# Performance work log

Hardware: AMD Instinct MI355X
Metric: run time of the kernel (lower is better)

Reference implementation:

```python
import jax, jax.numpy as jnp
import numpy as np

B, S, H = 1, 2048, 2048
NH, NKV, HD = 16, 2, 128
ROPE_THETA = 1000000.0
BF16 = jnp.bfloat16


def setup_inputs() -> dict:
    key = jax.random.key(0)
    ks = jax.random.split(key, 6)
    hidden_states = jax.random.normal(ks[0], (B, S, H), dtype=jnp.float32)
    # causal additive mask, 0 on/below diagonal, large negative above
    causal = jnp.tril(jnp.ones((S, S), dtype=bool))
    attention_mask = jnp.where(causal, 0.0, -1e9).astype(jnp.float32)[None, None, :, :]
    position_ids = jnp.arange(S, dtype=jnp.int32)[None, :]
    sc = 1.0 / np.sqrt(H)
    Wq = jax.random.normal(ks[1], (H, H), dtype=jnp.float32) * sc
    bq = jnp.zeros((H,), dtype=jnp.float32)
    Wk = jax.random.normal(ks[2], (H, NKV * HD), dtype=jnp.float32) * sc
    bk = jnp.zeros((NKV * HD,), dtype=jnp.float32)
    Wv = jax.random.normal(ks[3], (H, NKV * HD), dtype=jnp.float32) * sc
    bv = jnp.zeros((NKV * HD,), dtype=jnp.float32)
    Wo = jax.random.normal(ks[4], (H, H), dtype=jnp.float32) * sc
    return {"hidden_states": hidden_states, "attention_mask": attention_mask,
            "position_ids": position_ids, "Wq": Wq, "bq": bq, "Wk": Wk, "bk": bk,
            "Wv": Wv, "bv": bv, "Wo": Wo}


def _rope_tables(pos):
    # pos: [S] int. freqs: [HD//2]
    freqs = 1.0 / (ROPE_THETA ** (jnp.arange(0, HD, 2, dtype=jnp.float32) / HD))
    ang = pos.astype(jnp.float32)[:, None] * freqs[None, :]  # [S, HD//2]
    return jnp.cos(ang), jnp.sin(ang)


def _apply_rope(x, cos, sin):
    # x: [B,S,nheads,HD]; cos/sin: [S,HD//2] -> broadcast over heads
    c = cos[None, :, None, :]
    s = sin[None, :, None, :]
    x1, x2 = x[..., : HD // 2], x[..., HD // 2 :]
    return jnp.concatenate([x1 * c - x2 * s, x1 * s + x2 * c], axis=-1)


def reference(hidden_states, attention_mask, position_ids, Wq, bq, Wk, bk, Wv, bv, Wo):
    x = hidden_states.astype(BF16)
    # bf16 projections (flax Dense dtype=bfloat16)
    q = (x @ Wq.astype(BF16) + bq.astype(BF16)).reshape(B, S, NH, HD)
    k = (x @ Wk.astype(BF16) + bk.astype(BF16)).reshape(B, S, NKV, HD)
    v = (x @ Wv.astype(BF16) + bv.astype(BF16)).reshape(B, S, NKV, HD)
    cos, sin = _rope_tables(position_ids[0])
    q = _apply_rope(q.astype(jnp.float32), cos, sin).astype(jnp.float32)
    k = _apply_rope(k.astype(jnp.float32), cos, sin).astype(jnp.float32)
    cache_k, cache_v = k, v  # cache holds un-repeated kv (k post-rope, v bf16)
    rep = NH // NKV  # GQA repeat
    k = jnp.repeat(k, rep, axis=2)
    vr = jnp.repeat(v, rep, axis=2)
    # [B,NH,S,HD]
    qh = q.transpose(0, 2, 1, 3)
    kh = k.transpose(0, 2, 1, 3)
    vh = vr.transpose(0, 2, 1, 3).astype(jnp.float32)
    scale = 1.0 / jnp.sqrt(jnp.float32(HD))
    scores = jnp.einsum('bhqd,bhkd->bhqk', qh, kh) * scale + attention_mask
    probs = jnp.clip(jax.nn.softmax(scores.astype(jnp.float32), axis=-1), 1e-09, 1 - 1e-09)
    attn = jnp.einsum('bhqk,bhkd->bhqd', probs, vh)
    attn = attn.transpose(0, 2, 1, 3).reshape(B, S, H)
    out = (attn.astype(BF16) @ Wo.astype(BF16)).astype(jnp.float32)
    return out, cache_k, cache_v
```

## Files before the change

kernel.cpp:

```cpp
#include <hip/hip_runtime.h>
#include <hip/hip_bf16.h>
#include <math.h>

#define S_LEN 2048
#define HDIM  2048
#define N_H   16
#define N_KV  2
#define HD_   128
#define NQKV  2560

typedef __attribute__((ext_vector_type(8))) short bf16x8;
typedef __attribute__((ext_vector_type(4))) float f32x4;
typedef __attribute__((ext_vector_type(16))) float f32x16;

#define GLDS16(gsrc, ldst)                                                      \
  __builtin_amdgcn_global_load_lds(                                             \
      (const __attribute__((address_space(1))) void*)(gsrc),                    \
      (__attribute__((address_space(3))) void*)(ldst), 16, 0, 0)

__device__ __forceinline__ ushort f2b(float x) {
  union { __hip_bfloat16 b; ushort u; } c;
  c.b = __float2bfloat16(x);
  return c.u;
}
__device__ __forceinline__ float b2f(ushort u) {
  union { float f; unsigned v; } c;
  c.v = ((unsigned)u) << 16;
  return c.f;
}
__device__ __forceinline__ uint pk2(float a, float b) {
  return (uint)f2b(a) | ((uint)f2b(b) << 16);
}

__global__ __launch_bounds__(256) void k_f32_to_bf16(const float* __restrict__ src,
                                                     ushort* __restrict__ dst, int n4) {
  int i = blockIdx.x * 256 + threadIdx.x;
  if (i >= n4) return;
  float4 v = ((const float4*)src)[i];
  ushort4 o;
  o.x = f2b(v.x); o.y = f2b(v.y); o.z = f2b(v.z); o.w = f2b(v.w);
  ((ushort4*)dst)[i] = o;
}

__global__ __launch_bounds__(256) void k_transpose_bf16(const float* __restrict__ src,
                                                        ushort* __restrict__ dst,
                                                        int R, int C) {
  __shared__ float t[64][65];
  int c0 = blockIdx.x * 64, r0 = blockIdx.y * 64;
  int tx = threadIdx.x & 63, ty = threadIdx.x >> 6;
#pragma unroll
  for (int i = 0; i < 16; ++i)
    t[i * 4 + ty][tx] = src[(size_t)(r0 + i * 4 + ty) * C + (c0 + tx)];
  __syncthreads();
#pragma unroll
  for (int i = 0; i < 16; ++i)
    dst[(size_t)(c0 + i * 4 + ty) * R + (r0 + tx)] = f2b(t[tx][i * 4 + ty]);
}

__global__ __launch_bounds__(256) void k_gemm_bt(const ushort* __restrict__ A,
                                                 const ushort* __restrict__ Bt,
                                                 ushort* __restrict__ Cp,
                                                 int M, int N, int Kfull, int Khalf) {
  __shared__ ushort lA[128 * 32];
  __shared__ ushort lB[128 * 32];
  const int tid = threadIdx.x;
  const int w = tid >> 6, lane = tid & 63;
  const int lr = lane & 15, lg = lane >> 4;
  const int bm = blockIdx.x * 128, bn = blockIdx.y * 128;
  const int wm = (w >> 1) * 64, wn = (w & 1) * 64;
  const int kbeg = blockIdx.z * Khalf;
  ushort* Cout = Cp + (size_t)blockIdx.z * M * N;
  f32x4 acc[4][4] = {};

  for (int k0 = kbeg; k0 < kbeg + Khalf; k0 += 32) {
    __syncthreads();
#pragma unroll
    for (int it = 0; it < 2; ++it) {
      const int idx = it * 256 + tid;
      const int row = idx >> 2;
      const int kc = (idx & 3) * 8;
      GLDS16(A + (size_t)(bm + row) * Kfull + k0 + kc, lA + (it * 4 + w) * 512);
      GLDS16(Bt + (size_t)(bn + row) * Kfull + k0 + kc, lB + (it * 4 + w) * 512);
    }
    __syncthreads();
    bf16x8 af[4], bf[4];
#pragma unroll
    for (int i = 0; i < 4; ++i) {
      af[i] = *(const bf16x8*)(lA + (wm + i * 16 + lr) * 32 + lg * 8);
      bf[i] = *(const bf16x8*)(lB + (wn + i * 16 + lr) * 32 + lg * 8);
    }
    __builtin_amdgcn_s_setprio(1);
#pragma unroll
    for (int mi = 0; mi < 4; ++mi)
#pragma unroll
      for (int ni = 0; ni < 4; ++ni)
        acc[mi][ni] =
            __builtin_amdgcn_mfma_f32_16x16x32_bf16(af[mi], bf[ni], acc[mi][ni], 0, 0, 0);
    __builtin_amdgcn_s_setprio(0);
  }

#pragma unroll
  for (int mi = 0; mi < 4; ++mi)
#pragma unroll
    for (int ni = 0; ni < 4; ++ni)
#pragma unroll
      for (int r = 0; r < 4; ++r) {
        const int row = bm + wm + mi * 16 + lg * 4 + r;
        const int col = bn + wn + ni * 16 + lr;
        Cout[(size_t)row * N + col] = f2b(acc[mi][ni][r]);
      }
}

__global__ __launch_bounds__(256) void k_epirope(const ushort* __restrict__ p0,
                                                 const ushort* __restrict__ p1,
                                                 const float* __restrict__ bq,
                                                 const float* __restrict__ bk,
                                                 const float* __restrict__ bv,
                                                 const int* __restrict__ pos_ids,
                                                 ushort* __restrict__ q_r,
                                                 ushort* __restrict__ k_r,
                                                 ushort* __restrict__ v_t,
                                                 float* __restrict__ cache_k,
                                                 float* __restrict__ cache_v) {
  const int s = blockIdx.x;
  const int t = threadIdx.x;
  __shared__ float row[NQKV];
  const uint* a = (const uint*)(p0 + (size_t)s * NQKV);
  const uint* b = (const uint*)(p1 + (size_t)s * NQKV);
#pragma unroll
  for (int j = 0; j < 5; ++j) {
    const int c2 = t + 256 * j;
    const uint u0 = a[c2], u1 = b[c2];
    const int c = 2 * c2;
    const float v0 = b2f((ushort)u0) + b2f((ushort)(u1 & 0xffff));
    const float v1 = b2f((ushort)(u0 >> 16)) + b2f((ushort)(u1 >> 16));
    const float bias0 = (c < 2048) ? bq[c] : (c < 2304 ? bk[c - 2048] : bv[c - 2304]);
    const float bias1 = (c + 1 < 2048) ? bq[c + 1]
                                       : (c + 1 < 2304 ? bk[c + 1 - 2048] : bv[c + 1 - 2304]);
    row[c] = b2f(f2b(b2f(f2b(v0)) + b2f(f2b(bias0))));
    row[c + 1] = b2f(f2b(b2f(f2b(v1)) + b2f(f2b(bias1))));
  }
  __syncthreads();

  const int i = t & 63, g = t >> 6;
  const float SCALE = 0.08838834764831845f;
  const float pos = (float)pos_ids[s];
  const float freq = (float)(1.0 / pow(1000000.0, (double)i / 64.0));
  float sn, cs;
  sincosf(pos * freq, &sn, &cs);

#pragma unroll
  for (int j = 0; j < 4; ++j) {
    const int h = j * 4 + g;
    const float x1 = row[h * 128 + i];
    const float x2 = row[h * 128 + 64 + i];
    const float o1 = x1 * cs - x2 * sn;
    const float o2 = x1 * sn + x2 * cs;
    const size_t qo = ((size_t)h * S_LEN + s) * 128;
    q_r[qo + i] = f2b(o1 * SCALE);
    q_r[qo + 64 + i] = f2b(o2 * SCALE);
  }
  if (g < 2) {
    const int kv = g;
    const float x1 = row[2048 + kv * 128 + i];
    const float x2 = row[2048 + kv * 128 + 64 + i];
    const float o1 = x1 * cs - x2 * sn;
    const float o2 = x1 * sn + x2 * cs;
    const size_t ko = ((size_t)kv * S_LEN + s) * 128;
    k_r[ko + i] = f2b(o1);
    k_r[ko + 64 + i] = f2b(o2);
    const size_t co = ((size_t)s * 2 + kv) * 128;
    cache_k[co + i] = o1;
    cache_k[co + 64 + i] = o2;
  }
  {
    const int kv = t >> 7, d = t & 127;
    const float vval = row[2304 + kv * 128 + d];
    cache_v[((size_t)s * 2 + kv) * 128 + d] = vval;
    v_t[((size_t)kv * 128 + d) * S_LEN + s] = f2b(vval);
  }
}

__global__ __launch_bounds__(256) void k_addround(const ushort* __restrict__ p0,
                                                  const ushort* __restrict__ p1,
                                                  float* __restrict__ out, int n2) {
  int i = blockIdx.x * 256 + threadIdx.x;
  if (i >= n2) return;
  const uint a = ((const uint*)p0)[i];
  const uint b = ((const uint*)p1)[i];
  float2 o;
  o.x = b2f(f2b(b2f((ushort)(a & 0xffff)) + b2f((ushort)(b & 0xffff))));
  o.y = b2f(f2b(b2f((ushort)(a >> 16)) + b2f((ushort)(b >> 16))));
  ((float2*)out)[i] = o;
}

__global__ __launch_bounds__(256, 2) void k_attn(const ushort* __restrict__ q_r,
                                                 const ushort* __restrict__ k_r,
                                                 const ushort* __restrict__ v_t,
                                                 ushort* __restrict__ attn_b) {
  __shared__ ushort smem[2][2][8192];
  __shared__ float stats[2][32][2];

  const int bi = blockIdx.x;
  const int h = bi & 15;
  const int tq = (bi >> 4) & 15;
  const int Q = (bi >> 8) ? (31 - tq) : tq;
  const int kvh = h >> 3;

  const int tid = threadIdx.x, w = tid >> 6, lane = tid & 63;
  const int g = w >> 1, wq = w & 1, tg = tid & 127;
  const int l31 = lane & 31, hb = lane >> 5;
  const int S_steps = Q + 1;
  const int qmaxw = Q * 64 + wq * 32 + 31;

  bf16x8 qf[8];
  {
    const ushort* qp =
        q_r + ((size_t)(h * S_LEN + Q * 64 + wq * 32 + l31)) * 128 + hb * 8;
#pragma unroll
    for (int f = 0; f < 8; ++f) qf[f] = *(const bf16x8*)(qp + f * 16);
  }

  f32x16 acc[4] = {};
  float m = -INFINITY, l = 0.f;

#define STAGE(BUF, T32)                                                           \
  do {                                                                            \
    const int kb_ = (T32) * 32;                                                   \
    _Pragma("unroll") for (int i = 0; i < 4; ++i) {                               \
      const int idx = i * 128 + tg;                                               \
      {                                                                           \
        const int key = idx >> 4, sl = idx & 15;                                  \
        GLDS16(k_r + ((size_t)(kvh * S_LEN + kb_ + key)) * 128 +                  \
                   ((sl ^ (key & 7)) * 8),                                        \
               &smem[g][BUF][i * 1024 + wq * 512]);                               \
      }                                                                           \
      {                                                                           \
        const int d = idx >> 2, p = idx & 3;                                      \
        const int gs = (p - (d >> 1)) & 3;                                        \
        GLDS16(v_t + ((size_t)(kvh * HD_ + d)) * S_LEN + kb_ + gs * 8,            \
               &smem[g][BUF][4096 + i * 1024 + wq * 512]);                        \
      }                                                                           \
    }                                                                             \
  } while (0)

  STAGE(0, g);
  int buf = 0;

  for (int s = 0; s < S_steps; ++s) {
    __syncthreads();
    if (s + 1 < S_steps) STAGE(buf ^ 1, 2 * (s + 1) + g);
    const int kb = (2 * s + g) * 32;

    if (kb <= qmaxw) {
      const ushort* lK = &smem[g][buf][0];
      const ushort* lV = &smem[g][buf][4096];

      f32x16 p0 = {};
      __builtin_amdgcn_s_setprio(1);
#pragma unroll
      for (int f = 0; f < 8; ++f) {
        const int key = l31;
        const bf16x8 kf8 =
            *(const bf16x8*)(lK + key * 128 + (((2 * f + hb) ^ (key & 7)) * 8));
        p0 = __builtin_amdgcn_mfma_f32_32x32x16_bf16(kf8, qf[f], p0, 0, 0, 0);
      }
      __builtin_amdgcn_s_setprio(0);

      const int q = Q * 64 + wq * 32 + l31;
      float sv[16];
#pragma unroll
      for (int r = 0; r < 16; ++r) {
        const int key = kb + (r & 3) + 8 * (r >> 2) + 4 * hb;
        sv[r] = (key <= q) ? p0[r] : -INFINITY;
      }
      float t8[8];
#pragma unroll
      for (int j = 0; j < 8; ++j) t8[j] = fmaxf(sv[j], sv[j + 8]);
#pragma unroll
      for (int st = 4; st >= 1; st >>= 1)
#pragma unroll
        for (int j = 0; j < 4; ++j)
          if (j < st) t8[j] = fmaxf(t8[j], t8[j + st]);
      const float mxw = fmaxf(t8[0], __shfl_xor(t8[0], 32));

      if (__any(mxw > m + 8.f)) {
        const float mn = fmaxf(m, mxw);
        const float sc = __expf(m - mn);
#pragma unroll
        for (int g2 = 0; g2 < 4; ++g2)
#pragma unroll
          for (int r = 0; r < 16; ++r) acc[g2][r] *= sc;
        l *= sc;
        m = mn;
      }
#pragma unroll
      for (int r = 0; r < 16; ++r) sv[r] = __expf(sv[r] - m);
      float ts[8];
#pragma unroll
      for (int j = 0; j < 8; ++j) ts[j] = sv[j] + sv[j + 8];
#pragma unroll
      for (int st = 4; st >= 1; st >>= 1)
#pragma unroll
        for (int j = 0; j < 4; ++j)
          if (j < st) ts[j] += ts[j + st];
      l += ts[0];

      uint pk8[8];
#pragma unroll
      for (int j = 0; j < 8; ++j) pk8[j] = pk2(sv[2 * j], sv[2 * j + 1]);
      union FragU { uint wd[4]; bf16x8 v; };
      FragU frag[2];
#pragma unroll
      for (int c1 = 0; c1 < 2; ++c1) {
        uint mine0, mine1, rcv0, rcv1;
        {
          const uint pa = pk8[0 + 4 * c1];
          const uint pb = pk8[2 + 4 * c1];
          const uint mn_ = hb ? pb : pa;
          const uint xc_ = hb ? pa : pb;
          mine0 = mn_;
          rcv0 = (uint)__shfl_xor((int)xc_, 32);
        }
        {
          const uint pa = pk8[1 + 4 * c1];
          const uint pb = pk8[3 + 4 * c1];
          const uint mn_ = hb ? pb : pa;
          const uint xc_ = hb ? pa : pb;
          mine1 = mn_;
          rcv1 = (uint)__shfl_xor((int)xc_, 32);
        }
        frag[c1].wd[0] = hb ? rcv0 : mine0;
        frag[c1].wd[1] = hb ? rcv1 : mine1;
        frag[c1].wd[2] = hb ? mine0 : rcv0;
        frag[c1].wd[3] = hb ? mine1 : rcv1;
      }

      __builtin_amdgcn_s_setprio(1);
#pragma unroll
      for (int g2 = 0; g2 < 4; ++g2) {
        const int d = g2 * 32 + l31;
#pragma unroll
        for (int c = 0; c < 2; ++c) {
          const int phys = ((2 * c + hb) + (d >> 1)) & 3;
          const bf16x8 vf = *(const bf16x8*)(lV + d * 32 + phys * 8);
          acc[g2] = __builtin_amdgcn_mfma_f32_32x32x16_bf16(vf, frag[c].v, acc[g2], 0, 0, 0);
        }
      }
      __builtin_amdgcn_s_setprio(0);
    }
    buf ^= 1;
  }
  __syncthreads();

  float* mrg = (float*)&smem[0][0][0];
  float* ldsO = (float*)&smem[1][0][0];
  if (g == 1) {
    const float lt1 = l + __shfl_xor(l, 32);
#pragma unroll
    for (int g2 = 0; g2 < 4; ++g2)
#pragma unroll
      for (int r = 0; r < 16; ++r) {
        const int d5 = (r & 3) + 8 * (r >> 2) + 4 * hb;
        mrg[wq * 4096 + (g2 * 32 + d5) * 32 + l31] = acc[g2][r];
      }
    if (hb == 0) {
      stats[wq][l31][0] = m;
      stats[wq][l31][1] = lt1;
    }
  }
  __syncthreads();
  if (g == 0) {
    const float m1 = stats[wq][l31][0];
    const float l1 = stats[wq][l31][1];
    const float l0 = l + __shfl_xor(l, 32);
    const float ms = fmaxf(m, m1);
    const float f0 = __expf(m - ms);
    const float f1 = __expf(m1 - ms);
    const float inv = 1.0f / (l0 * f0 + l1 * f1);
#pragma unroll
    for (int g2 = 0; g2 < 4; ++g2)
#pragma unroll
      for (int r = 0; r < 16; ++r) {
        const int d5 = (r & 3) + 8 * (r >> 2) + 4 * hb;
        const float o1v = mrg[wq * 4096 + (g2 * 32 + d5) * 32 + l31];
        const float val = (acc[g2][r] * f0 + o1v * f1) * inv;
        ldsO[wq * 4096 + l31 * 128 + g2 * 32 + (d5 ^ l31)] = val;
      }
#pragma unroll
    for (int pass = 0; pass < 8; ++pass) {
      const int qrow = pass * 4 + (lane >> 4);
      const int d0 = (lane & 15) * 8;
      float v[8];
#pragma unroll
      for (int j = 0; j < 8; ++j)
        v[j] = ldsO[wq * 4096 + qrow * 128 + (((d0 + j) & 31) ^ qrow) + (d0 & 96)];
      uint4 o;
      o.x = pk2(v[0], v[1]); o.y = pk2(v[2], v[3]);
      o.z = pk2(v[4], v[5]); o.w = pk2(v[6], v[7]);
      const size_t qg = (size_t)(Q * 64 + wq * 32 + qrow);
      *(uint4*)(attn_b + qg * HDIM + h * 128 + d0) = o;
    }
  }
#undef STAGE
}

extern "C" void kernel_launch(void* const* d_in, const int* in_sizes, int n_in,
                              void* d_out, int out_size, void* d_ws, size_t ws_size,
                              hipStream_t stream) {
  const float* hidden = (const float*)d_in[0];
  const int* pos_ids = (const int*)d_in[2];
  const float* Wq = (const float*)d_in[3];
  const float* bq = (const float*)d_in[4];
  const float* Wk = (const float*)d_in[5];
  const float* bk = (const float*)d_in[6];
  const float* Wv = (const float*)d_in[7];
  const float* bv = (const float*)d_in[8];
  const float* Wo = (const float*)d_in[9];

  float* out = (float*)d_out;
  float* cache_k = out + (size_t)S_LEN * HDIM;
  float* cache_v = cache_k + (size_t)S_LEN * N_KV * HD_;

  char* ws = (char*)d_ws;
  ushort* x_b = (ushort*)(ws);
  ushort* wt = (ushort*)(ws + (8ull << 20));
  ushort* qkvp = (ushort*)(ws + (18ull << 20));
  ushort* wo_t = (ushort*)(ws);
  ushort* q_r = (ushort*)(ws + (8ull << 20));
  ushort* k_r = (ushort*)(ws + (16ull << 20));
  ushort* v_t = (ushort*)(ws + (17ull << 20));
  ushort* attn_b = (ushort*)(ws + (18ull << 20));
  ushort* outp = (ushort*)(ws + (26ull << 20));

  k_f32_to_bf16<<<dim3((S_LEN * HDIM) / 1024), 256, 0, stream>>>(hidden, x_b,
                                                                 (S_LEN * HDIM) / 4);
  k_transpose_bf16<<<dim3(32, 32), 256, 0, stream>>>(Wq, wt, 2048, 2048);
  k_transpose_bf16<<<dim3(4, 32), 256, 0, stream>>>(Wk, wt + (size_t)2048 * 2048, 2048, 256);
  k_transpose_bf16<<<dim3(4, 32), 256, 0, stream>>>(Wv, wt + (size_t)2304 * 2048, 2048, 256);
  k_gemm_bt<<<dim3(16, 20, 2), 256, 0, stream>>>(x_b, wt, qkvp, 2048, 2560, 2048, 1024);
  k_transpose_bf16<<<dim3(32, 32), 256, 0, stream>>>(Wo, wo_t, 2048, 2048);
  k_epirope<<<dim3(S_LEN), 256, 0, stream>>>(qkvp, qkvp + (size_t)2048 * 2560, bq, bk, bv,
                                             pos_ids, q_r, k_r, v_t, cache_k, cache_v);
  k_attn<<<dim3(512), 256, 0, stream>>>(q_r, k_r, v_t, attn_b);
  k_gemm_bt<<<dim3(16, 16, 2), 256, 0, stream>>>(attn_b, wo_t, outp, 2048, 2048, 2048, 1024);
  k_addround<<<dim3((2048 * 2048 / 2 + 255) / 256), 256, 0, stream>>>(
      outp, outp + (size_t)2048 * 2048, out, 2048 * 2048 / 2);
}
```

Baseline: 158.9 us.

## Split causal attention KV range into chunks with separate merge kernel

Query tiles beyond the first eight are split into KV chunks of eight steps each, so each block handles a bounded amount of work. Partial unnormalized outputs go to workspace in bf16, with per-row max and sum in fp32, and a new merge kernel combines them with log-sum-exp weights. This raises the attention grid from 512 to 1280 blocks to balance the uneven causal workload. The QK dot product is also split into two independent MFMA accumulator chains to shorten the dependency chain. The cost is an extra kernel launch, extra workspace traffic, and an added bf16 rounding of the partial outputs.

```diff
diff --git a/kernel.cpp b/kernel.cpp
--- a/kernel.cpp
+++ b/kernel.cpp
@@ -197,20 +197,27 @@
 __global__ __launch_bounds__(256, 2) void k_attn(const ushort* __restrict__ q_r,
                                                  const ushort* __restrict__ k_r,
                                                  const ushort* __restrict__ v_t,
-                                                 ushort* __restrict__ attn_b) {
+                                                 ushort* __restrict__ attn_b,
+                                                 ushort* __restrict__ pO,
+                                                 float* __restrict__ pML) {
   __shared__ ushort smem[2][2][8192];
   __shared__ float stats[2][32][2];
 
   const int bi = blockIdx.x;
   const int h = bi & 15;
-  const int tq = (bi >> 4) & 15;
-  const int Q = (bi >> 8) ? (31 - tq) : tq;
+  const int j = bi >> 4;
+  const int b = (j < 8) ? 0 : (j < 24) ? 1 : (j < 48) ? 2 : 3;
+  const int rr = j - 4 * b * (b + 1);
+  const int Q = 8 * b + rr / (b + 1);
+  const int cch = rr % (b + 1);
+  const int s_beg = 8 * cch;
+  const int s_end = min(8 * cch + 8, Q + 1);
+  const bool single = (b == 0);
   const int kvh = h >> 3;
 
   const int tid = threadIdx.x, w = tid >> 6, lane = tid & 63;
   const int g = w >> 1, wq = w & 1, tg = tid & 127;
   const int l31 = lane & 31, hb = lane >> 5;
-  const int S_steps = Q + 1;
   const int qmaxw = Q * 64 + wq * 32 + 31;
 
   bf16x8 qf[8];
@@ -244,28 +251,36 @@
     }                                                                             \
   } while (0)
 
-  STAGE(0, g);
+  STAGE(0, 2 * s_beg + g);
   int buf = 0;
 
-  for (int s = 0; s < S_steps; ++s) {
+  for (int s = s_beg; s < s_end; ++s) {
     __syncthreads();
-    if (s + 1 < S_steps) STAGE(buf ^ 1, 2 * (s + 1) + g);
+    if (s + 1 < s_end) STAGE(buf ^ 1, 2 * (s + 1) + g);
     const int kb = (2 * s + g) * 32;
 
     if (kb <= qmaxw) {
       const ushort* lK = &smem[g][buf][0];
       const ushort* lV = &smem[g][buf][4096];
 
-      f32x16 p0 = {};
+      f32x16 pa = {}, pb = {};
       __builtin_amdgcn_s_setprio(1);
 #pragma unroll
-      for (int f = 0; f < 8; ++f) {
+      for (int f = 0; f < 4; ++f) {
         const int key = l31;
         const bf16x8 kf8 =
             *(const bf16x8*)(lK + key * 128 + (((2 * f + hb) ^ (key & 7)) * 8));
-        p0 = __builtin_amdgcn_mfma_f32_32x32x16_bf16(kf8, qf[f], p0, 0, 0, 0);
+        pa = __builtin_amdgcn_mfma_f32_32x32x16_bf16(kf8, qf[f], pa, 0, 0, 0);
+      }
+#pragma unroll
+      for (int f = 4; f < 8; ++f) {
+        const int key = l31;
+        const bf16x8 kf8 =
+            *(const bf16x8*)(lK + key * 128 + (((2 * f + hb) ^ (key & 7)) * 8));
+        pb = __builtin_amdgcn_mfma_f32_32x32x16_bf16(kf8, qf[f], pb, 0, 0, 0);
       }
       __builtin_amdgcn_s_setprio(0);
+      const f32x16 p0 = pa + pb;
 
       const int q = Q * 64 + wq * 32 + l31;
       float sv[16];
@@ -276,12 +291,12 @@
       }
       float t8[8];
 #pragma unroll
-      for (int j = 0; j < 8; ++j) t8[j] = fmaxf(sv[j], sv[j + 8]);
+      for (int jj = 0; jj < 8; ++jj) t8[jj] = fmaxf(sv[jj], sv[jj + 8]);
 #pragma unroll
       for (int st = 4; st >= 1; st >>= 1)
 #pragma unroll
-        for (int j = 0; j < 4; ++j)
-          if (j < st) t8[j] = fmaxf(t8[j], t8[j + st]);
+        for (int jj = 0; jj < 4; ++jj)
+          if (jj < st) t8[jj] = fmaxf(t8[jj], t8[jj + st]);
       const float mxw = fmaxf(t8[0], __shfl_xor(t8[0], 32));
 
       if (__any(mxw > m + 8.f)) {
@@ -298,35 +313,35 @@
       for (int r = 0; r < 16; ++r) sv[r] = __expf(sv[r] - m);
       float ts[8];
 #pragma unroll
-      for (int j = 0; j < 8; ++j) ts[j] = sv[j] + sv[j + 8];
+      for (int jj = 0; jj < 8; ++jj) ts[jj] = sv[jj] + sv[jj + 8];
 #pragma unroll
       for (int st = 4; st >= 1; st >>= 1)
 #pragma unroll
-        for (int j = 0; j < 4; ++j)
-          if (j < st) ts[j] += ts[j + st];
+        for (int jj = 0; jj < 4; ++jj)
+          if (jj < st) ts[jj] += ts[jj + st];
       l += ts[0];
 
       uint pk8[8];
 #pragma unroll
-      for (int j = 0; j < 8; ++j) pk8[j] = pk2(sv[2 * j], sv[2 * j + 1]);
+      for (int jj = 0; jj < 8; ++jj) pk8[jj] = pk2(sv[2 * jj], sv[2 * jj + 1]);
       union FragU { uint wd[4]; bf16x8 v; };
       FragU frag[2];
 #pragma unroll
       for (int c1 = 0; c1 < 2; ++c1) {
         uint mine0, mine1, rcv0, rcv1;
         {
-          const uint pa = pk8[0 + 4 * c1];
-          const uint pb = pk8[2 + 4 * c1];
-          const uint mn_ = hb ? pb : pa;
-          const uint xc_ = hb ? pa : pb;
+          const uint pa_ = pk8[0 + 4 * c1];
+          const uint pb_ = pk8[2 + 4 * c1];
+          const uint mn_ = hb ? pb_ : pa_;
+          const uint xc_ = hb ? pa_ : pb_;
           mine0 = mn_;
           rcv0 = (uint)__shfl_xor((int)xc_, 32);
         }
         {
-          const uint pa = pk8[1 + 4 * c1];
-          const uint pb = pk8[3 + 4 * c1];
-          const uint mn_ = hb ? pb : pa;
-          const uint xc_ = hb ? pa : pb;
+          const uint pa_ = pk8[1 + 4 * c1];
+          const uint pb_ = pk8[3 + 4 * c1];
+          const uint mn_ = hb ? pb_ : pa_;
+          const uint xc_ = hb ? pa_ : pb_;
           mine1 = mn_;
           rcv1 = (uint)__shfl_xor((int)xc_, 32);
         }
@@ -371,13 +386,15 @@
   }
   __syncthreads();
   if (g == 0) {
+    const int slot = h * 72 + (j - 8);
     const float m1 = stats[wq][l31][0];
     const float l1 = stats[wq][l31][1];
     const float l0 = l + __shfl_xor(l, 32);
     const float ms = fmaxf(m, m1);
     const float f0 = __expf(m - ms);
     const float f1 = __expf(m1 - ms);
-    const float inv = 1.0f / (l0 * f0 + l1 * f1);
+    const float Lc = l0 * f0 + l1 * f1;
+    const float inv = single ? 1.0f / Lc : 1.0f;
 #pragma unroll
     for (int g2 = 0; g2 < 4; ++g2)
 #pragma unroll
@@ -387,22 +404,81 @@
         const float val = (acc[g2][r] * f0 + o1v * f1) * inv;
         ldsO[wq * 4096 + l31 * 128 + g2 * 32 + (d5 ^ l31)] = val;
       }
+    if (!single && hb == 0) {
+      pML[(size_t)slot * 128 + (wq * 32 + l31) * 2] = ms;
+      pML[(size_t)slot * 128 + (wq * 32 + l31) * 2 + 1] = Lc;
+    }
 #pragma unroll
     for (int pass = 0; pass < 8; ++pass) {
       const int qrow = pass * 4 + (lane >> 4);
       const int d0 = (lane & 15) * 8;
       float v[8];
 #pragma unroll
-      for (int j = 0; j < 8; ++j)
-        v[j] = ldsO[wq * 4096 + qrow * 128 + (((d0 + j) & 31) ^ qrow) + (d0 & 96)];
+      for (int jj = 0; jj < 8; ++jj)
+        v[jj] = ldsO[wq * 4096 + qrow * 128 + (((d0 + jj) & 31) ^ qrow) + (d0 & 96)];
       uint4 o;
       o.x = pk2(v[0], v[1]); o.y = pk2(v[2], v[3]);
       o.z = pk2(v[4], v[5]); o.w = pk2(v[6], v[7]);
-      const size_t qg = (size_t)(Q * 64 + wq * 32 + qrow);
-      *(uint4*)(attn_b + qg * HDIM + h * 128 + d0) = o;
+      if (single) {
+        const size_t qg = (size_t)(Q * 64 + wq * 32 + qrow);
+        *(uint4*)(attn_b + qg * HDIM + h * 128 + d0) = o;
+      } else {
+        *(uint4*)(pO + (size_t)slot * 8192 + (wq * 32 + qrow) * 128 + d0) = o;
+      }
     }
   }
 #undef STAGE
+}
+
+__global__ __launch_bounds__(256) void k_attn_merge(const ushort* __restrict__ pO,
+                                                    const float* __restrict__ pML,
+                                                    ushort* __restrict__ attn_b) {
+  const int bi = blockIdx.x;
+  const int h = bi / 24, Q = 8 + bi % 24;
+  const int b = Q >> 3;
+  const int off = (b == 1) ? (Q - 8) * 2 : (b == 2) ? 16 + (Q - 16) * 3 : 40 + (Q - 24) * 4;
+  const int P = b + 1;
+  const int base = h * 72 + off;
+  const int q = threadIdx.x >> 2, seg = (threadIdx.x & 3) * 32;
+
+  const float* mlb = pML + (size_t)base * 128 + q * 2;
+  const float m0 = mlb[0], l0 = mlb[1];
+  const float m1 = mlb[128], l1 = mlb[129];
+  const float m2 = (P > 2) ? mlb[256] : -INFINITY;
+  const float l2 = (P > 2) ? mlb[257] : 0.f;
+  const float m3 = (P > 3) ? mlb[384] : -INFINITY;
+  const float l3 = (P > 3) ? mlb[385] : 0.f;
+  const float ms = fmaxf(fmaxf(m0, m1), fmaxf(m2, m3));
+  const float w0 = __expf(m0 - ms), w1 = __expf(m1 - ms);
+  const float w2 = (P > 2) ? __expf(m2 - ms) : 0.f;
+  const float w3 = (P > 3) ? __expf(m3 - ms) : 0.f;
+  const float inv = 1.0f / (l0 * w0 + l1 * w1 + l2 * w2 + l3 * w3);
+
+  const ushort* po = pO + (size_t)base * 8192 + q * 128;
+  ushort* dst = attn_b + (size_t)(Q * 64 + q) * HDIM + h * 128;
+
+#define ACC8(PTR, W)                                                    \
+  {                                                                     \
+    const uint4 v = *(const uint4*)(PTR);                               \
+    o0 += b2f((ushort)(v.x & 0xffff)) * (W); o1 += b2f((ushort)(v.x >> 16)) * (W); \
+    o2 += b2f((ushort)(v.y & 0xffff)) * (W); o3 += b2f((ushort)(v.y >> 16)) * (W); \
+    o4 += b2f((ushort)(v.z & 0xffff)) * (W); o5 += b2f((ushort)(v.z >> 16)) * (W); \
+    o6 += b2f((ushort)(v.w & 0xffff)) * (W); o7 += b2f((ushort)(v.w >> 16)) * (W); \
+  }
+#pragma unroll
+  for (int u = 0; u < 4; ++u) {
+    const int d = seg + u * 8;
+    float o0 = 0, o1 = 0, o2 = 0, o3 = 0, o4 = 0, o5 = 0, o6 = 0, o7 = 0;
+    ACC8(po + d, w0);
+    ACC8(po + 8192 + d, w1);
+    if (P > 2) ACC8(po + 2 * 8192 + d, w2);
+    if (P > 3) ACC8(po + 3 * 8192 + d, w3);
+    uint4 ov;
+    ov.x = pk2(o0 * inv, o1 * inv); ov.y = pk2(o2 * inv, o3 * inv);
+    ov.z = pk2(o4 * inv, o5 * inv); ov.w = pk2(o6 * inv, o7 * inv);
+    *(uint4*)(dst + d) = ov;
+  }
+#undef ACC8
 }
 
 extern "C" void kernel_launch(void* const* d_in, const int* in_sizes, int n_in,
@@ -431,6 +507,8 @@
   ushort* k_r = (ushort*)(ws + (16ull << 20));
   ushort* v_t = (ushort*)(ws + (17ull << 20));
   ushort* attn_b = (ushort*)(ws + (18ull << 20));
+  ushort* pO = (ushort*)(ws + (26ull << 20));
+  float* pML = (float*)(ws + (45ull << 20));
   ushort* outp = (ushort*)(ws + (26ull << 20));
 
   k_f32_to_bf16<<<dim3((S_LEN * HDIM) / 1024), 256, 0, stream>>>(hidden, x_b,
@@ -442,7 +520,8 @@
   k_transpose_bf16<<<dim3(32, 32), 256, 0, stream>>>(Wo, wo_t, 2048, 2048);
   k_epirope<<<dim3(S_LEN), 256, 0, stream>>>(qkvp, qkvp + (size_t)2048 * 2560, bq, bk, bv,
                                              pos_ids, q_r, k_r, v_t, cache_k, cache_v);
-  k_attn<<<dim3(512), 256, 0, stream>>>(q_r, k_r, v_t, attn_b);
+  k_attn<<<dim3(1280), 256, 0, stream>>>(q_r, k_r, v_t, attn_b, pO, pML);
+  k_attn_merge<<<dim3(384), 256, 0, stream>>>(pO, pML, attn_b);
   k_gemm_bt<<<dim3(16, 16, 2), 256, 0, stream>>>(attn_b, wo_t, outp, 2048, 2048, 2048, 1024);
   k_addround<<<dim3((2048 * 2048 / 2 + 255) / 256), 256, 0, stream>>>(
       outp, outp + (size_t)2048 * 2048, out, 2048 * 2048 / 2);
```

New measurement: 167.5 us. 5.4% more time.

## Fuse prep kernels into one launch and shrink GEMM M-tile to 64

Applied to the files above, without the earlier changes.

The hidden-state bf16 conversion and the Wq/Wk/Wv transposes are merged into a single kernel with a block-index dispatch, replacing four launches with one. The GEMM tile shrinks from 128x128 to 64x128, doubling grid size for better CU occupancy on the QKV and output projections. Workspace offsets are rearranged so the Wo transpose no longer overlaps buffers still in use. The smaller tiles mean less data reuse per block, so more global/LDS traffic per FLOP.

```diff
diff --git a/kernel.cpp b/kernel.cpp
--- a/kernel.cpp
+++ b/kernel.cpp
@@ -32,14 +32,43 @@
   return (uint)f2b(a) | ((uint)f2b(b) << 16);
 }
 
-__global__ __launch_bounds__(256) void k_f32_to_bf16(const float* __restrict__ src,
-                                                     ushort* __restrict__ dst, int n4) {
-  int i = blockIdx.x * 256 + threadIdx.x;
-  if (i >= n4) return;
-  float4 v = ((const float4*)src)[i];
-  ushort4 o;
-  o.x = f2b(v.x); o.y = f2b(v.y); o.z = f2b(v.z); o.w = f2b(v.w);
-  ((ushort4*)dst)[i] = o;
+__global__ __launch_bounds__(256) void k_prep(const float* __restrict__ hidden,
+                                              const float* __restrict__ Wq,
+                                              const float* __restrict__ Wk,
+                                              const float* __restrict__ Wv,
+                                              ushort* __restrict__ x_b,
+                                              ushort* __restrict__ wt) {
+  __shared__ float t[64][65];
+  const int bid = blockIdx.x;
+  const int tid = threadIdx.x;
+  if (bid < 4096) {
+    const int i = bid * 256 + tid;
+    float4 v = ((const float4*)hidden)[i];
+    ushort4 o;
+    o.x = f2b(v.x); o.y = f2b(v.y); o.z = f2b(v.z); o.w = f2b(v.w);
+    ((ushort4*)x_b)[i] = o;
+    return;
+  }
+  int tb = bid - 4096;
+  const float* src;
+  ushort* dst;
+  int C, bx, by;
+  if (tb < 1024) {
+    src = Wq; dst = wt; C = 2048; bx = tb & 31; by = tb >> 5;
+  } else if (tb < 1152) {
+    tb -= 1024; src = Wk; dst = wt + (size_t)2048 * 2048; C = 256; bx = tb & 3; by = tb >> 2;
+  } else {
+    tb -= 1152; src = Wv; dst = wt + (size_t)2304 * 2048; C = 256; bx = tb & 3; by = tb >> 2;
+  }
+  const int c0 = bx * 64, r0 = by * 64;
+  const int tx = tid & 63, ty = tid >> 6;
+#pragma unroll
+  for (int i = 0; i < 16; ++i)
+    t[i * 4 + ty][tx] = src[(size_t)(r0 + i * 4 + ty) * C + (c0 + tx)];
+  __syncthreads();
+#pragma unroll
+  for (int i = 0; i < 16; ++i)
+    dst[(size_t)(c0 + i * 4 + ty) * 2048 + (r0 + tx)] = f2b(t[tx][i * 4 + ty]);
 }
 
 __global__ __launch_bounds__(256) void k_transpose_bf16(const float* __restrict__ src,
@@ -61,37 +90,42 @@
                                                  const ushort* __restrict__ Bt,
                                                  ushort* __restrict__ Cp,
                                                  int M, int N, int Kfull, int Khalf) {
-  __shared__ ushort lA[128 * 32];
+  __shared__ ushort lA[64 * 32];
   __shared__ ushort lB[128 * 32];
   const int tid = threadIdx.x;
   const int w = tid >> 6, lane = tid & 63;
   const int lr = lane & 15, lg = lane >> 4;
-  const int bm = blockIdx.x * 128, bn = blockIdx.y * 128;
-  const int wm = (w >> 1) * 64, wn = (w & 1) * 64;
+  const int bm = blockIdx.x * 64, bn = blockIdx.y * 128;
+  const int wr = (w >> 1) * 32, wc = (w & 1) * 64;
   const int kbeg = blockIdx.z * Khalf;
   ushort* Cout = Cp + (size_t)blockIdx.z * M * N;
-  f32x4 acc[4][4] = {};
+  f32x4 acc[2][4] = {};
 
   for (int k0 = kbeg; k0 < kbeg + Khalf; k0 += 32) {
     __syncthreads();
+    {
+      const int row = tid >> 2;
+      const int kc = (tid & 3) * 8;
+      GLDS16(A + (size_t)(bm + row) * Kfull + k0 + kc, lA + w * 512);
+    }
 #pragma unroll
     for (int it = 0; it < 2; ++it) {
       const int idx = it * 256 + tid;
       const int row = idx >> 2;
       const int kc = (idx & 3) * 8;
-      GLDS16(A + (size_t)(bm + row) * Kfull + k0 + kc, lA + (it * 4 + w) * 512);
       GLDS16(Bt + (size_t)(bn + row) * Kfull + k0 + kc, lB + (it * 4 + w) * 512);
     }
     __syncthreads();
-    bf16x8 af[4], bf[4];
-#pragma unroll
-    for (int i = 0; i < 4; ++i) {
-      af[i] = *(const bf16x8*)(lA + (wm + i * 16 + lr) * 32 + lg * 8);
-      bf[i] = *(const bf16x8*)(lB + (wn + i * 16 + lr) * 32 + lg * 8);
-    }
+    bf16x8 af[2], bf[4];
+#pragma unroll
+    for (int i = 0; i < 2; ++i)
+      af[i] = *(const bf16x8*)(lA + (wr + i * 16 + lr) * 32 + lg * 8);
+#pragma unroll
+    for (int i = 0; i < 4; ++i)
+      bf[i] = *(const bf16x8*)(lB + (wc + i * 16 + lr) * 32 + lg * 8);
     __builtin_amdgcn_s_setprio(1);
 #pragma unroll
-    for (int mi = 0; mi < 4; ++mi)
+    for (int mi = 0; mi < 2; ++mi)
 #pragma unroll
       for (int ni = 0; ni < 4; ++ni)
         acc[mi][ni] =
@@ -100,13 +134,13 @@
   }
 
 #pragma unroll
-  for (int mi = 0; mi < 4; ++mi)
+  for (int mi = 0; mi < 2; ++mi)
 #pragma unroll
     for (int ni = 0; ni < 4; ++ni)
 #pragma unroll
       for (int r = 0; r < 4; ++r) {
-        const int row = bm + wm + mi * 16 + lg * 4 + r;
-        const int col = bn + wn + ni * 16 + lr;
+        const int row = bm + wr + mi * 16 + lg * 4 + r;
+        const int col = bn + wc + ni * 16 + lr;
         Cout[(size_t)row * N + col] = f2b(acc[mi][ni][r]);
       }
 }
@@ -315,18 +349,18 @@
       for (int c1 = 0; c1 < 2; ++c1) {
         uint mine0, mine1, rcv0, rcv1;
         {
-          const uint pa = pk8[0 + 4 * c1];
-          const uint pb = pk8[2 + 4 * c1];
-          const uint mn_ = hb ? pb : pa;
-          const uint xc_ = hb ? pa : pb;
+          const uint pa_ = pk8[0 + 4 * c1];
+          const uint pb_ = pk8[2 + 4 * c1];
+          const uint mn_ = hb ? pb_ : pa_;
+          const uint xc_ = hb ? pa_ : pb_;
           mine0 = mn_;
           rcv0 = (uint)__shfl_xor((int)xc_, 32);
         }
         {
-          const uint pa = pk8[1 + 4 * c1];
-          const uint pb = pk8[3 + 4 * c1];
-          const uint mn_ = hb ? pb : pa;
-          const uint xc_ = hb ? pa : pb;
+          const uint pa_ = pk8[1 + 4 * c1];
+          const uint pb_ = pk8[3 + 4 * c1];
+          const uint mn_ = hb ? pb_ : pa_;
+          const uint xc_ = hb ? pa_ : pb_;
           mine1 = mn_;
           rcv1 = (uint)__shfl_xor((int)xc_, 32);
         }
@@ -426,24 +460,20 @@
   ushort* x_b = (ushort*)(ws);
   ushort* wt = (ushort*)(ws + (8ull << 20));
   ushort* qkvp = (ushort*)(ws + (18ull << 20));
-  ushort* wo_t = (ushort*)(ws);
-  ushort* q_r = (ushort*)(ws + (8ull << 20));
-  ushort* k_r = (ushort*)(ws + (16ull << 20));
-  ushort* v_t = (ushort*)(ws + (17ull << 20));
+  ushort* q_r = (ushort*)(ws);
+  ushort* k_r = (ushort*)(ws + (8ull << 20));
+  ushort* v_t = (ushort*)(ws + (9ull << 20));
+  ushort* wo_t = (ushort*)(ws + (10ull << 20));
   ushort* attn_b = (ushort*)(ws + (18ull << 20));
   ushort* outp = (ushort*)(ws + (26ull << 20));
 
-  k_f32_to_bf16<<<dim3((S_LEN * HDIM) / 1024), 256, 0, stream>>>(hidden, x_b,
-                                                                 (S_LEN * HDIM) / 4);
-  k_transpose_bf16<<<dim3(32, 32), 256, 0, stream>>>(Wq, wt, 2048, 2048);
-  k_transpose_bf16<<<dim3(4, 32), 256, 0, stream>>>(Wk, wt + (size_t)2048 * 2048, 2048, 256);
-  k_transpose_bf16<<<dim3(4, 32), 256, 0, stream>>>(Wv, wt + (size_t)2304 * 2048, 2048, 256);
-  k_gemm_bt<<<dim3(16, 20, 2), 256, 0, stream>>>(x_b, wt, qkvp, 2048, 2560, 2048, 1024);
+  k_prep<<<dim3(5376), 256, 0, stream>>>(hidden, Wq, Wk, Wv, x_b, wt);
+  k_gemm_bt<<<dim3(32, 20, 2), 256, 0, stream>>>(x_b, wt, qkvp, 2048, 2560, 2048, 1024);
   k_transpose_bf16<<<dim3(32, 32), 256, 0, stream>>>(Wo, wo_t, 2048, 2048);
   k_epirope<<<dim3(S_LEN), 256, 0, stream>>>(qkvp, qkvp + (size_t)2048 * 2560, bq, bk, bv,
                                              pos_ids, q_r, k_r, v_t, cache_k, cache_v);
   k_attn<<<dim3(512), 256, 0, stream>>>(q_r, k_r, v_t, attn_b);
-  k_gemm_bt<<<dim3(16, 16, 2), 256, 0, stream>>>(attn_b, wo_t, outp, 2048, 2048, 2048, 1024);
+  k_gemm_bt<<<dim3(32, 16, 2), 256, 0, stream>>>(attn_b, wo_t, outp, 2048, 2048, 2048, 1024);
   k_addround<<<dim3((2048 * 2048 / 2 + 255) / 256), 256, 0, stream>>>(
       outp, outp + (size_t)2048 * 2048, out, 2048 * 2048 / 2);
 }
```

After: 162.1 us. No clear change (+2.0%).
